# Performance work log

Hardware: AMD Instinct MI355X
Metric: run time of the kernel (lower is better)

## Reference

```python
import jax, jax.numpy as jnp
import numpy as np

N_NODES = 100000
N_EDGES = 1200000
IN_CH = 64


def setup_inputs() -> dict:
    key = jax.random.key(0)
    ks = jax.random.split(key, 6)
    scale = 1.0 / np.sqrt(IN_CH)
    return {
        "x": jax.random.normal(ks[0], (N_NODES, IN_CH), dtype=jnp.float32),
        "edge_index": jax.random.randint(ks[1], (2, N_EDGES), 0, N_NODES, dtype=jnp.int64),
        "W_gcn": jax.random.normal(ks[2], (IN_CH, IN_CH), dtype=jnp.float32) * scale,
        "b_gcn": jnp.zeros((IN_CH,), dtype=jnp.float32),
        "W1": jax.random.normal(ks[3], (IN_CH, 32), dtype=jnp.float32) * scale,
        "b1": jnp.zeros((32,), dtype=jnp.float32),
        "W2": jax.random.normal(ks[4], (32, 32), dtype=jnp.float32) * (1.0 / np.sqrt(32)),
        "b2": jnp.zeros((32,), dtype=jnp.float32),
        "W3": jax.random.normal(ks[5], (32, 2), dtype=jnp.float32) * (1.0 / np.sqrt(32)),
        "b3": jnp.zeros((2,), dtype=jnp.float32),
    }


def _gcn_conv(x, edge_index, W, b):
    # PyG GCNConv: add self-loops, symmetric normalization D^-1/2 A D^-1/2 (X W) + b
    N = x.shape[0]
    loop = jnp.arange(N, dtype=edge_index.dtype)
    src = jnp.concatenate([edge_index[0], loop])
    dst = jnp.concatenate([edge_index[1], loop])
    deg = jax.ops.segment_sum(jnp.ones_like(dst, dtype=x.dtype), dst, num_segments=N)
    d_inv_sqrt = jax.lax.rsqrt(deg)  # deg >= 1 thanks to self-loops
    norm = d_inv_sqrt[src] * d_inv_sqrt[dst]  # [E+N]
    h = x @ W  # [N, C]
    msg = h[src] * norm[:, None]  # gather + scale, [E+N, C]
    agg = jax.ops.segment_sum(msg, dst, num_segments=N)  # scatter-add, [N, C]
    return agg + b


def reference(x, edge_index, W_gcn, b_gcn, W1, b1, W2, b2, W3, b3):
    out = jax.nn.relu(_gcn_conv(x, edge_index, W_gcn, b_gcn))
    h = out + x  # residual
    h = jax.nn.relu(h @ W1 + b1)
    h = jax.nn.relu(h @ W2 + b2)
    return h @ W3 + b3  # [N, 2]
```

## Files before the change

### kernel.cpp

```cpp
#include <hip/hip_runtime.h>

#define NN 100000
#define CH 64
#define CAP 64
#define NPART 8
#define PSIZE ((NN + NPART - 1) / NPART)
#define FILLB 640

__device__ __forceinline__ float bf_lo(unsigned u) { return __uint_as_float(u << 16); }
__device__ __forceinline__ float bf_hi(unsigned u) { return __uint_as_float(u & 0xffff0000u); }

__device__ __forceinline__ unsigned short f2bf(float f) {
    unsigned u = __float_as_uint(f);
    u += 0x7fffu + ((u >> 16) & 1u);
    return (unsigned short)(u >> 16);
}

__global__ __launch_bounds__(256) void k_fill(const int* __restrict__ src,
                                              const int* __restrict__ dst,
                                              unsigned* __restrict__ cnt,
                                              int* __restrict__ bsrc, int E) {
    int part = blockIdx.x & (NPART - 1);
    int blk  = blockIdx.x >> 3;
    int lo = part * PSIZE, hi = lo + PSIZE;
    int E4 = E >> 2;
    const int4* src4 = (const int4*)src;
    const int4* dst4 = (const int4*)dst;
    for (int i = blk * 256 + threadIdx.x; i < E4; i += FILLB * 256) {
        int4 d4 = dst4[i];
        int4 s4 = src4[i];
        if (d4.x >= lo && d4.x < hi) { unsigned p = atomicAdd(&cnt[d4.x], 1u); if (p < CAP) bsrc[(size_t)d4.x * CAP + p] = s4.x; }
        if (d4.y >= lo && d4.y < hi) { unsigned p = atomicAdd(&cnt[d4.y], 1u); if (p < CAP) bsrc[(size_t)d4.y * CAP + p] = s4.y; }
        if (d4.z >= lo && d4.z < hi) { unsigned p = atomicAdd(&cnt[d4.z], 1u); if (p < CAP) bsrc[(size_t)d4.z * CAP + p] = s4.z; }
        if (d4.w >= lo && d4.w < hi) { unsigned p = atomicAdd(&cnt[d4.w], 1u); if (p < CAP) bsrc[(size_t)d4.w * CAP + p] = s4.w; }
    }
    if (part == 0 && blk == 0) {
        for (int e = E4 * 4 + threadIdx.x; e < E; e += 256) {
            int d = dst[e];
            int s = src[e];
            unsigned p = atomicAdd(&cnt[d], 1u);
            if (p < CAP) bsrc[(size_t)d * CAP + p] = s;
        }
    }
}

__global__ __launch_bounds__(256) void k_prep(const float* __restrict__ x,
                                              unsigned short* __restrict__ xb,
                                              const unsigned* __restrict__ cnt,
                                              float* __restrict__ dinv, int N) {
    int i = blockIdx.x * blockDim.x + threadIdx.x;
    int tot4 = N * CH / 4;
    if (i < tot4) {
        float4 v = ((const float4*)x)[i];
        ushort4 o;
        o.x = f2bf(v.x); o.y = f2bf(v.y); o.z = f2bf(v.z); o.w = f2bf(v.w);
        ((ushort4*)xb)[i] = o;
    }
    if (i < N) dinv[i] = rsqrtf((float)cnt[i] + 1.0f);
}

__global__ __launch_bounds__(256) void k_at(
        const unsigned* __restrict__ cnt, const int* __restrict__ bsrc,
        const float* __restrict__ dinv, const float* __restrict__ x,
        const unsigned short* __restrict__ xb,
        const float* __restrict__ Wg, const float* __restrict__ bgcn,
        const float* __restrict__ W1, const float* __restrict__ b1,
        const float* __restrict__ W2, const float* __restrict__ b2,
        const float* __restrict__ W3, const float* __restrict__ b3,
        float* __restrict__ out, int N) {
    __shared__ float R1[4096];
    __shared__ float R2[32 * 65];
    __shared__ float R3[32 * 33];
    __shared__ float bgs[64];
    int t = threadIdx.x;
    int nbase = blockIdx.x * 32;

    for (int i = t; i < 4096; i += 256) R1[i] = Wg[i];
    if (t < 64) bgs[t] = bgcn[t];

    {
        int nl = t >> 3, o = t & 7;
        int n = nbase + nl;
        float* r2p = R2 + nl * 65 + o * 8;
        if (n < N) {
            int c = (int)cnt[n]; if (c > CAP) c = CAP;
            const int* bp = bsrc + (size_t)n * CAP;
            float dn = dinv[n];
            float acc[8];
#pragma unroll
            for (int j = 0; j < 8; ++j) acc[j] = 0.f;
#pragma unroll 4
            for (int e = 0; e < c; ++e) {
                int s = bp[e];
                float w = dinv[s];
                uint4 A = ((const uint4*)(xb + (size_t)s * CH))[o];
                acc[0] += bf_lo(A.x) * w; acc[1] += bf_hi(A.x) * w;
                acc[2] += bf_lo(A.y) * w; acc[3] += bf_hi(A.y) * w;
                acc[4] += bf_lo(A.z) * w; acc[5] += bf_hi(A.z) * w;
                acc[6] += bf_lo(A.w) * w; acc[7] += bf_hi(A.w) * w;
            }
            const float4* xq = (const float4*)(x + (size_t)n * CH);
            float4 u0 = xq[2 * o], u1 = xq[2 * o + 1];
            r2p[0] = dn * (acc[0] + u0.x * dn); r2p[1] = dn * (acc[1] + u0.y * dn);
            r2p[2] = dn * (acc[2] + u0.z * dn); r2p[3] = dn * (acc[3] + u0.w * dn);
            r2p[4] = dn * (acc[4] + u1.x * dn); r2p[5] = dn * (acc[5] + u1.y * dn);
            r2p[6] = dn * (acc[6] + u1.z * dn); r2p[7] = dn * (acc[7] + u1.w * dn);
        } else {
#pragma unroll
            for (int j = 0; j < 8; ++j) r2p[j] = 0.f;
        }
    }
    __syncthreads();

    int cg = t & 15, ng = t >> 4;
    float accv[2][4];
#pragma unroll
    for (int i = 0; i < 2; ++i)
#pragma unroll
        for (int u = 0; u < 4; ++u) accv[i][u] = 0.f;
#pragma unroll 4
    for (int k = 0; k < 64; ++k) {
        float wv0 = R1[k * 64 + cg * 4 + 0];
        float wv1 = R1[k * 64 + cg * 4 + 1];
        float wv2 = R1[k * 64 + cg * 4 + 2];
        float wv3 = R1[k * 64 + cg * 4 + 3];
        float va = R2[(ng * 2 + 0) * 65 + k];
        float vb = R2[(ng * 2 + 1) * 65 + k];
        accv[0][0] += va * wv0; accv[0][1] += va * wv1; accv[0][2] += va * wv2; accv[0][3] += va * wv3;
        accv[1][0] += vb * wv0; accv[1][1] += vb * wv1; accv[1][2] += vb * wv2; accv[1][3] += vb * wv3;
    }
    __syncthreads();

    for (int i = t; i < 2048; i += 256) R1[i] = W1[i];
    for (int i = t; i < 1024; i += 256) R1[2048 + i] = W2[i];
    if (t < 64) R1[3072 + t] = W3[t];
    if (t < 32) { R1[3136 + t] = b1[t]; R1[3168 + t] = b2[t]; }
    if (t < 2) R1[3200 + t] = b3[t];
#pragma unroll
    for (int i = 0; i < 2; ++i) {
        int nl2 = ng * 2 + i;
        int gr = nbase + nl2;
        float4 xv = make_float4(0.f, 0.f, 0.f, 0.f);
        if (gr < N) xv = *((const float4*)(x + (size_t)gr * CH) + cg);
        float* rp = R2 + nl2 * 65 + cg * 4;
        rp[0] = fmaxf(accv[i][0] + bgs[cg * 4 + 0], 0.f) + xv.x;
        rp[1] = fmaxf(accv[i][1] + bgs[cg * 4 + 1], 0.f) + xv.y;
        rp[2] = fmaxf(accv[i][2] + bgs[cg * 4 + 2], 0.f) + xv.z;
        rp[3] = fmaxf(accv[i][3] + bgs[cg * 4 + 3], 0.f) + xv.w;
    }
    __syncthreads();

    int nl = t & 31, g2 = t >> 5;
    {
        float a[4];
#pragma unroll
        for (int j = 0; j < 4; ++j) a[j] = R1[3136 + 4 * g2 + j];
#pragma unroll 4
        for (int k = 0; k < 64; ++k) {
            float v = R2[nl * 65 + k];
#pragma unroll
            for (int j = 0; j < 4; ++j)
                a[j] += v * R1[k * 32 + 4 * g2 + j];
        }
#pragma unroll
        for (int j = 0; j < 4; ++j) R3[nl * 33 + 4 * g2 + j] = a[j];
    }
    __syncthreads();

    {
        float a[4];
#pragma unroll
        for (int j = 0; j < 4; ++j) a[j] = R1[3168 + 4 * g2 + j];
#pragma unroll 4
        for (int k = 0; k < 32; ++k) {
            float v = fmaxf(R3[nl * 33 + k], 0.0f);
#pragma unroll
            for (int j = 0; j < 4; ++j)
                a[j] += v * R1[2048 + k * 32 + 4 * g2 + j];
        }
#pragma unroll
        for (int j = 0; j < 4; ++j) R2[nl * 65 + 4 * g2 + j] = a[j];
    }
    __syncthreads();

    if (t < 64) {
        int nl4 = t >> 1, g4 = t & 1;
        int gr = nbase + nl4;
        if (gr < N) {
            float y = R1[3200 + g4];
#pragma unroll
            for (int k = 0; k < 32; ++k)
                y += fmaxf(R2[nl4 * 65 + k], 0.0f) * R1[3072 + k * 2 + g4];
            out[(size_t)gr * 2 + g4] = y;
        }
    }
}

extern "C" void kernel_launch(void* const* d_in, const int* in_sizes, int n_in,
                              void* d_out, int out_size, void* d_ws, size_t ws_size,
                              hipStream_t stream) {
    const float* x  = (const float*)d_in[0];
    const int*   ei = (const int*)d_in[1];
    const float* Wg = (const float*)d_in[2];
    const float* bg = (const float*)d_in[3];
    const float* W1 = (const float*)d_in[4];
    const float* b1 = (const float*)d_in[5];
    const float* W2 = (const float*)d_in[6];
    const float* b2 = (const float*)d_in[7];
    const float* W3 = (const float*)d_in[8];
    const float* b3 = (const float*)d_in[9];
    float* out = (float*)d_out;

    const int N = NN;
    const int E = in_sizes[1] / 2;
    const int* src = ei;
    const int* dst = ei + E;

    char* base = (char*)d_ws;
    size_t o = 0;
    auto alloc = [&](size_t bytes) { void* p = base + o; o = (o + bytes + 255) & ~(size_t)255; return p; };
    unsigned*       cnt  = (unsigned*)alloc((size_t)N * 4);
    float*          dinv = (float*)alloc((size_t)N * 4);
    int*            bsrc = (int*)alloc((size_t)N * CAP * 4);
    unsigned short* xb   = (unsigned short*)alloc((size_t)N * CH * 2);

    hipMemsetAsync(cnt, 0, (size_t)N * 4, stream);

    k_fill<<<NPART * FILLB, 256, 0, stream>>>(src, dst, cnt, bsrc, E);
    int prep_blocks = (N * CH / 4 + 255) / 256;
    k_prep<<<prep_blocks, 256, 0, stream>>>(x, xb, cnt, dinv, N);
    k_at<<<(N + 31) / 32, 256, 0, stream>>>(cnt, bsrc, dinv, x, xb, Wg, bg,
                                            W1, b1, W2, b2, W3, b3, out, N);
}
```

Measured before the change: 208.1 us.

## Fuse bf16 conversion into fill kernel, compute rsqrt inline, halve node tile

Moves the x-to-bf16 conversion into the edge-bucketing kernel and removes the separate prep kernel and dinv buffer. The degree normalisation is now recomputed in the aggregation kernel from cnt with rsqrt on each gather. The aggregation kernel now handles 16 nodes per block with 16 threads per node, each loading 8 bytes, so there are twice as many blocks with more lanes per row. This saves one launch and a pass over memory, but adds a per-edge rsqrt, doubles how often each block loads the weight matrices, and makes each gather load narrower.

```diff
diff --git a/kernel.cpp b/kernel.cpp
--- a/kernel.cpp
+++ b/kernel.cpp
@@ -18,15 +18,19 @@
 
 __global__ __launch_bounds__(256) void k_fill(const int* __restrict__ src,
                                               const int* __restrict__ dst,
+                                              const float* __restrict__ x,
                                               unsigned* __restrict__ cnt,
-                                              int* __restrict__ bsrc, int E) {
+                                              int* __restrict__ bsrc,
+                                              unsigned short* __restrict__ xb,
+                                              int E, int N) {
+    int t = threadIdx.x;
     int part = blockIdx.x & (NPART - 1);
     int blk  = blockIdx.x >> 3;
     int lo = part * PSIZE, hi = lo + PSIZE;
     int E4 = E >> 2;
     const int4* src4 = (const int4*)src;
     const int4* dst4 = (const int4*)dst;
-    for (int i = blk * 256 + threadIdx.x; i < E4; i += FILLB * 256) {
+    for (int i = blk * 256 + t; i < E4; i += FILLB * 256) {
         int4 d4 = dst4[i];
         int4 s4 = src4[i];
         if (d4.x >= lo && d4.x < hi) { unsigned p = atomicAdd(&cnt[d4.x], 1u); if (p < CAP) bsrc[(size_t)d4.x * CAP + p] = s4.x; }
@@ -35,99 +39,76 @@
         if (d4.w >= lo && d4.w < hi) { unsigned p = atomicAdd(&cnt[d4.w], 1u); if (p < CAP) bsrc[(size_t)d4.w * CAP + p] = s4.w; }
     }
     if (part == 0 && blk == 0) {
-        for (int e = E4 * 4 + threadIdx.x; e < E; e += 256) {
+        for (int e = E4 * 4 + t; e < E; e += 256) {
             int d = dst[e];
             int s = src[e];
             unsigned p = atomicAdd(&cnt[d], 1u);
             if (p < CAP) bsrc[(size_t)d * CAP + p] = s;
         }
     }
-}
-
-__global__ __launch_bounds__(256) void k_prep(const float* __restrict__ x,
-                                              unsigned short* __restrict__ xb,
-                                              const unsigned* __restrict__ cnt,
-                                              float* __restrict__ dinv, int N) {
-    int i = blockIdx.x * blockDim.x + threadIdx.x;
     int tot4 = N * CH / 4;
-    if (i < tot4) {
+    for (int i = blockIdx.x * 256 + t; i < tot4; i += NPART * FILLB * 256) {
         float4 v = ((const float4*)x)[i];
         ushort4 o;
         o.x = f2bf(v.x); o.y = f2bf(v.y); o.z = f2bf(v.z); o.w = f2bf(v.w);
         ((ushort4*)xb)[i] = o;
     }
-    if (i < N) dinv[i] = rsqrtf((float)cnt[i] + 1.0f);
 }
 
 __global__ __launch_bounds__(256) void k_at(
         const unsigned* __restrict__ cnt, const int* __restrict__ bsrc,
-        const float* __restrict__ dinv, const float* __restrict__ x,
-        const unsigned short* __restrict__ xb,
+        const float* __restrict__ x, const unsigned short* __restrict__ xb,
         const float* __restrict__ Wg, const float* __restrict__ bgcn,
         const float* __restrict__ W1, const float* __restrict__ b1,
         const float* __restrict__ W2, const float* __restrict__ b2,
         const float* __restrict__ W3, const float* __restrict__ b3,
         float* __restrict__ out, int N) {
     __shared__ float R1[4096];
-    __shared__ float R2[32 * 65];
-    __shared__ float R3[32 * 33];
+    __shared__ float R2[16 * 65];
+    __shared__ float R3[16 * 33];
     __shared__ float bgs[64];
     int t = threadIdx.x;
-    int nbase = blockIdx.x * 32;
+    int nbase = blockIdx.x * 16;
 
     for (int i = t; i < 4096; i += 256) R1[i] = Wg[i];
     if (t < 64) bgs[t] = bgcn[t];
 
-    {
-        int nl = t >> 3, o = t & 7;
+    int nl = t >> 4, o = t & 15;
+    {
         int n = nbase + nl;
-        float* r2p = R2 + nl * 65 + o * 8;
+        float* r2p = R2 + nl * 65 + o * 4;
         if (n < N) {
-            int c = (int)cnt[n]; if (c > CAP) c = CAP;
+            int craw = (int)cnt[n];
+            int c = craw > CAP ? CAP : craw;
+            float dn = rsqrtf((float)craw + 1.0f);
             const int* bp = bsrc + (size_t)n * CAP;
-            float dn = dinv[n];
-            float acc[8];
-#pragma unroll
-            for (int j = 0; j < 8; ++j) acc[j] = 0.f;
+            float a0 = 0.f, a1 = 0.f, a2 = 0.f, a3 = 0.f;
 #pragma unroll 4
             for (int e = 0; e < c; ++e) {
                 int s = bp[e];
-                float w = dinv[s];
-                uint4 A = ((const uint4*)(xb + (size_t)s * CH))[o];
-                acc[0] += bf_lo(A.x) * w; acc[1] += bf_hi(A.x) * w;
-                acc[2] += bf_lo(A.y) * w; acc[3] += bf_hi(A.y) * w;
-                acc[4] += bf_lo(A.z) * w; acc[5] += bf_hi(A.z) * w;
-                acc[6] += bf_lo(A.w) * w; acc[7] += bf_hi(A.w) * w;
+                float w = rsqrtf((float)cnt[s] + 1.0f);
+                uint2 A = ((const uint2*)(xb + (size_t)s * CH))[o];
+                a0 += bf_lo(A.x) * w; a1 += bf_hi(A.x) * w;
+                a2 += bf_lo(A.y) * w; a3 += bf_hi(A.y) * w;
             }
-            const float4* xq = (const float4*)(x + (size_t)n * CH);
-            float4 u0 = xq[2 * o], u1 = xq[2 * o + 1];
-            r2p[0] = dn * (acc[0] + u0.x * dn); r2p[1] = dn * (acc[1] + u0.y * dn);
-            r2p[2] = dn * (acc[2] + u0.z * dn); r2p[3] = dn * (acc[3] + u0.w * dn);
-            r2p[4] = dn * (acc[4] + u1.x * dn); r2p[5] = dn * (acc[5] + u1.y * dn);
-            r2p[6] = dn * (acc[6] + u1.z * dn); r2p[7] = dn * (acc[7] + u1.w * dn);
+            float4 u = ((const float4*)(x + (size_t)n * CH))[o];
+            r2p[0] = dn * (a0 + u.x * dn);
+            r2p[1] = dn * (a1 + u.y * dn);
+            r2p[2] = dn * (a2 + u.z * dn);
+            r2p[3] = dn * (a3 + u.w * dn);
         } else {
-#pragma unroll
-            for (int j = 0; j < 8; ++j) r2p[j] = 0.f;
-        }
-    }
-    __syncthreads();
-
-    int cg = t & 15, ng = t >> 4;
-    float accv[2][4];
-#pragma unroll
-    for (int i = 0; i < 2; ++i)
-#pragma unroll
-        for (int u = 0; u < 4; ++u) accv[i][u] = 0.f;
+            r2p[0] = 0.f; r2p[1] = 0.f; r2p[2] = 0.f; r2p[3] = 0.f;
+        }
+    }
+    __syncthreads();
+
+    int cg = o, ng = nl;
+    float av[4] = {0.f, 0.f, 0.f, 0.f};
 #pragma unroll 4
     for (int k = 0; k < 64; ++k) {
-        float wv0 = R1[k * 64 + cg * 4 + 0];
-        float wv1 = R1[k * 64 + cg * 4 + 1];
-        float wv2 = R1[k * 64 + cg * 4 + 2];
-        float wv3 = R1[k * 64 + cg * 4 + 3];
-        float va = R2[(ng * 2 + 0) * 65 + k];
-        float vb = R2[(ng * 2 + 1) * 65 + k];
-        accv[0][0] += va * wv0; accv[0][1] += va * wv1; accv[0][2] += va * wv2; accv[0][3] += va * wv3;
-        accv[1][0] += vb * wv0; accv[1][1] += vb * wv1; accv[1][2] += vb * wv2; accv[1][3] += vb * wv3;
+        float4 wv = ((const float4*)(R1 + k * 64))[cg];
+        float v = R2[ng * 65 + k];
+        av[0] += v * wv.x; av[1] += v * wv.y; av[2] += v * wv.z; av[3] += v * wv.w;
     }
     __syncthreads();
 
@@ -136,54 +117,46 @@
     if (t < 64) R1[3072 + t] = W3[t];
     if (t < 32) { R1[3136 + t] = b1[t]; R1[3168 + t] = b2[t]; }
     if (t < 2) R1[3200 + t] = b3[t];
-#pragma unroll
-    for (int i = 0; i < 2; ++i) {
-        int nl2 = ng * 2 + i;
-        int gr = nbase + nl2;
+    {
+        int gr = nbase + ng;
         float4 xv = make_float4(0.f, 0.f, 0.f, 0.f);
         if (gr < N) xv = *((const float4*)(x + (size_t)gr * CH) + cg);
-        float* rp = R2 + nl2 * 65 + cg * 4;
-        rp[0] = fmaxf(accv[i][0] + bgs[cg * 4 + 0], 0.f) + xv.x;
-        rp[1] = fmaxf(accv[i][1] + bgs[cg * 4 + 1], 0.f) + xv.y;
-        rp[2] = fmaxf(accv[i][2] + bgs[cg * 4 + 2], 0.f) + xv.z;
-        rp[3] = fmaxf(accv[i][3] + bgs[cg * 4 + 3], 0.f) + xv.w;
-    }
-    __syncthreads();
-
-    int nl = t & 31, g2 = t >> 5;
-    {
-        float a[4];
-#pragma unroll
-        for (int j = 0; j < 4; ++j) a[j] = R1[3136 + 4 * g2 + j];
+        float* rp = R2 + ng * 65 + cg * 4;
+        rp[0] = fmaxf(av[0] + bgs[cg * 4 + 0], 0.f) + xv.x;
+        rp[1] = fmaxf(av[1] + bgs[cg * 4 + 1], 0.f) + xv.y;
+        rp[2] = fmaxf(av[2] + bgs[cg * 4 + 2], 0.f) + xv.z;
+        rp[3] = fmaxf(av[3] + bgs[cg * 4 + 3], 0.f) + xv.w;
+    }
+    __syncthreads();
+
+    int nl2 = t & 15, g2 = t >> 4;
+    {
+        float a0 = R1[3136 + 2 * g2], a1 = R1[3136 + 2 * g2 + 1];
 #pragma unroll 4
         for (int k = 0; k < 64; ++k) {
-            float v = R2[nl * 65 + k];
-#pragma unroll
-            for (int j = 0; j < 4; ++j)
-                a[j] += v * R1[k * 32 + 4 * g2 + j];
-        }
-#pragma unroll
-        for (int j = 0; j < 4; ++j) R3[nl * 33 + 4 * g2 + j] = a[j];
-    }
-    __syncthreads();
-
-    {
-        float a[4];
-#pragma unroll
-        for (int j = 0; j < 4; ++j) a[j] = R1[3168 + 4 * g2 + j];
+            float v = R2[nl2 * 65 + k];
+            a0 += v * R1[k * 32 + 2 * g2];
+            a1 += v * R1[k * 32 + 2 * g2 + 1];
+        }
+        R3[nl2 * 33 + 2 * g2]     = a0;
+        R3[nl2 * 33 + 2 * g2 + 1] = a1;
+    }
+    __syncthreads();
+
+    {
+        float a0 = R1[3168 + 2 * g2], a1 = R1[3168 + 2 * g2 + 1];
 #pragma unroll 4
         for (int k = 0; k < 32; ++k) {
-            float v = fmaxf(R3[nl * 33 + k], 0.0f);
-#pragma unroll
-            for (int j = 0; j < 4; ++j)
-                a[j] += v * R1[2048 + k * 32 + 4 * g2 + j];
-        }
-#pragma unroll
-        for (int j = 0; j < 4; ++j) R2[nl * 65 + 4 * g2 + j] = a[j];
-    }
-    __syncthreads();
-
-    if (t < 64) {
+            float v = fmaxf(R3[nl2 * 33 + k], 0.0f);
+            a0 += v * R1[2048 + k * 32 + 2 * g2];
+            a1 += v * R1[2048 + k * 32 + 2 * g2 + 1];
+        }
+        R2[nl2 * 65 + 2 * g2]     = a0;
+        R2[nl2 * 65 + 2 * g2 + 1] = a1;
+    }
+    __syncthreads();
+
+    if (t < 32) {
         int nl4 = t >> 1, g4 = t & 1;
         int gr = nbase + nl4;
         if (gr < N) {
@@ -220,15 +193,12 @@
     size_t o = 0;
     auto alloc = [&](size_t bytes) { void* p = base + o; o = (o + bytes + 255) & ~(size_t)255; return p; };
     unsigned*       cnt  = (unsigned*)alloc((size_t)N * 4);
-    float*          dinv = (float*)alloc((size_t)N * 4);
     int*            bsrc = (int*)alloc((size_t)N * CAP * 4);
     unsigned short* xb   = (unsigned short*)alloc((size_t)N * CH * 2);
 
     hipMemsetAsync(cnt, 0, (size_t)N * 4, stream);
 
-    k_fill<<<NPART * FILLB, 256, 0, stream>>>(src, dst, cnt, bsrc, E);
-    int prep_blocks = (N * CH / 4 + 255) / 256;
-    k_prep<<<prep_blocks, 256, 0, stream>>>(x, xb, cnt, dinv, N);
-    k_at<<<(N + 31) / 32, 256, 0, stream>>>(cnt, bsrc, dinv, x, xb, Wg, bg,
+    k_fill<<<NPART * FILLB, 256, 0, stream>>>(src, dst, x, cnt, bsrc, xb, E, N);
+    k_at<<<(N + 15) / 16, 256, 0, stream>>>(cnt, bsrc, x, xb, Wg, bg,
                                             W1, b1, W2, b2, W3, b3, out, N);
 }
```

After: 219.8 us. 5.6% more time.
